# Performance work log

Hardware: AMD Instinct MI355X
Metric: run time of the kernel (lower is better)

The kernel has to match this reference:

```python
import jax, jax.numpy as jnp
import numpy as np
from jax import lax

N_EMBD = 4096
N_EXPERTS = 64


def setup_inputs() -> dict:
    key = jax.random.key(0)
    kx, kw = jax.random.split(key)
    x = jax.random.normal(kx, (4, 4096, N_EMBD), dtype=jnp.float32)
    # nn.Linear(n_embd, n_experts, bias=False) -> weight shape [n_experts, n_embd]
    W = jax.random.normal(kw, (N_EXPERTS, N_EMBD), dtype=jnp.float32) * (1.0 / np.sqrt(N_EMBD))
    return {"x": x, "W": W}


def reference(x, W):
    # logits = x @ W^T : [B, S, n_experts]
    logits = jnp.einsum('bsd,ed->bse', x, W)
    topk_vals, topk_idx = lax.top_k(logits, 2)  # [B, S, 2]
    gates = jax.nn.softmax(topk_vals, axis=-1)  # softmax over just the top-2 values
    return (topk_idx, gates)
```

## Files before the change

kernel.cpp:

```cpp
#include <hip/hip_runtime.h>
#include <math.h>

#define N_EMBD    4096
#define N_EXPERTS 64
#define N_TOKENS  16384
#define TAU       1e-3f
#define NT_BLK    32
#define KS        4
#define K_BLK     (N_EMBD / KS)
#define NT2       16

typedef __attribute__((ext_vector_type(8))) short bf16x8;
typedef __attribute__((ext_vector_type(4))) float f32x4;

#define MFMA16 __builtin_amdgcn_mfma_f32_16x16x32_bf16
#define PIN2(a, b) asm volatile("" :: "v"(a), "v"(b))

struct hl_pair { unsigned h, l; };

__device__ __forceinline__ hl_pair split_pair(float f0, float f1) {
    unsigned u0 = __builtin_bit_cast(unsigned, f0);
    unsigned u1 = __builtin_bit_cast(unsigned, f1);
    unsigned r0 = u0 + 0x7FFFu + ((u0 >> 16) & 1u);
    unsigned r1 = u1 + 0x7FFFu + ((u1 >> 16) & 1u);
    hl_pair p;
    p.h = (r0 >> 16) | (r1 & 0xFFFF0000u);
    float h0 = __builtin_bit_cast(float, r0 & 0xFFFF0000u);
    float h1 = __builtin_bit_cast(float, r1 & 0xFFFF0000u);
    float l0 = f0 - h0;
    float l1 = f1 - h1;
    unsigned v0 = __builtin_bit_cast(unsigned, l0);
    unsigned v1 = __builtin_bit_cast(unsigned, l1);
    unsigned s0 = v0 + 0x7FFFu + ((v0 >> 16) & 1u);
    unsigned s1 = v1 + 0x7FFFu + ((v1 >> 16) & 1u);
    p.l = (s0 >> 16) | (s1 & 0xFFFF0000u);
    return p;
}

__global__ void w_pack_bf16(const float* __restrict__ W,
                            uint4* __restrict__ Bpack,
                            int* __restrict__ flags) {
    int tid = blockIdx.x * blockDim.x + threadIdx.x;
    if (tid == 0) flags[0] = 0;
    int lane = tid & 63;
    int nt   = (tid >> 6) & 3;
    int ks   = tid >> 8;
    int e = nt * 16 + (lane & 15);
    int k = ks * 32 + ((lane >> 4) << 3);
    const float* src = W + (size_t)e * N_EMBD + k;
    uint4 hp, lp;
    hl_pair p0 = split_pair(src[0], src[1]);
    hl_pair p1 = split_pair(src[2], src[3]);
    hl_pair p2 = split_pair(src[4], src[5]);
    hl_pair p3 = split_pair(src[6], src[7]);
    hp.x = p0.h; lp.x = p0.l;
    hp.y = p1.h; lp.y = p1.l;
    hp.z = p2.h; lp.z = p2.l;
    hp.w = p3.h; lp.w = p3.l;
    size_t F = (size_t)ks * 8 + nt * 2;
    Bpack[F * 64 + lane]       = hp;
    Bpack[(F + 1) * 64 + lane] = lp;
}

__device__ __forceinline__ void store_split8(char* buf, int off, f32x4 a, f32x4 b) {
    hl_pair p0 = split_pair(a.x, a.y);
    hl_pair p1 = split_pair(a.z, a.w);
    hl_pair p2 = split_pair(b.x, b.y);
    hl_pair p3 = split_pair(b.z, b.w);
    uint4 h, l;
    h.x = p0.h; h.y = p1.h; h.z = p2.h; h.w = p3.h;
    l.x = p0.l; l.y = p1.l; l.z = p2.l; l.w = p3.l;
    *(uint4*)(buf + off)        = h;
    *(uint4*)(buf + off + 4096) = l;
}

__global__ __launch_bounds__(256, 4) void router_gemm(
        const float* __restrict__ x,
        const uint4* __restrict__ Bpack,
        float* __restrict__ partial) {
    __shared__ __align__(16) char ldsA[2 * 8192];

    const int tid  = threadIdx.x;
    const int lane = tid & 63;
    const int w    = tid >> 6;
    const int kq   = blockIdx.x & 3;
    const int tok0 = (blockIdx.x >> 2) * NT_BLK;
    const int l15 = lane & 15, l16 = lane >> 4;

    const int row_w = tid >> 3;
    const int c8    = tid & 7;
    const f32x4* g = (const f32x4*)(x + (size_t)(tok0 + row_w) * N_EMBD
                                      + kq * K_BLK + c8 * 8);
    const int wo = row_w * 128 + ((c8 * 16) ^ ((row_w & 7) << 4));

    const int swz_r = (l15 & 7) << 4;
    const int ro0 = l15 * 128 + ((l16 * 16)      ^ swz_r);
    const int ro1 = l15 * 128 + ((64 + l16 * 16) ^ swz_r);

    f32x4 acc0 = {0.f, 0.f, 0.f, 0.f};
    f32x4 acc1 = {0.f, 0.f, 0.f, 0.f};
    f32x4 ra0, ra1, rb0, rb1;

    char* buf0 = ldsA;
    char* buf1 = ldsA + 8192;

    const uint4* bbase = Bpack + ((size_t)(kq * 32) * 8 + w * 2) * 64 + lane;

#define LOADA(P, t) { P##0 = g[(t) * 16]; P##1 = g[(t) * 16 + 1]; }
#define STOREA(buf, P) store_split8(buf, wo, P##0, P##1)
#define COMPUTE(bufR, tt) {                                                   \
    const uint4* bq = bbase + (size_t)(tt) * 1024;                            \
    uint4 bh0q = bq[0];   uint4 bl0q = bq[64];                                \
    uint4 bh1q = bq[512]; uint4 bl1q = bq[576];                               \
    bf16x8 bh0 = __builtin_bit_cast(bf16x8, bh0q);                            \
    bf16x8 bl0 = __builtin_bit_cast(bf16x8, bl0q);                            \
    bf16x8 bh1 = __builtin_bit_cast(bf16x8, bh1q);                            \
    bf16x8 bl1 = __builtin_bit_cast(bf16x8, bl1q);                            \
    bf16x8 a;                                                                 \
    a = *(const bf16x8*)((bufR) + ro0);                                       \
    acc0 = MFMA16(a, bh0, acc0, 0, 0, 0);                                     \
    acc0 = MFMA16(a, bl0, acc0, 0, 0, 0);                                     \
    a = *(const bf16x8*)((bufR) + ro0 + 4096);                                \
    acc0 = MFMA16(a, bh0, acc0, 0, 0, 0);                                     \
    a = *(const bf16x8*)((bufR) + ro0 + 2048);                                \
    acc1 = MFMA16(a, bh0, acc1, 0, 0, 0);                                     \
    acc1 = MFMA16(a, bl0, acc1, 0, 0, 0);                                     \
    a = *(const bf16x8*)((bufR) + ro0 + 2048 + 4096);                         \
    acc1 = MFMA16(a, bh0, acc1, 0, 0, 0);                                     \
    a = *(const bf16x8*)((bufR) + ro1);                                       \
    acc0 = MFMA16(a, bh1, acc0, 0, 0, 0);                                     \
    acc0 = MFMA16(a, bl1, acc0, 0, 0, 0);                                     \
    a = *(const bf16x8*)((bufR) + ro1 + 4096);                                \
    acc0 = MFMA16(a, bh1, acc0, 0, 0, 0);                                     \
    a = *(const bf16x8*)((bufR) + ro1 + 2048);                                \
    acc1 = MFMA16(a, bh1, acc1, 0, 0, 0);                                     \
    acc1 = MFMA16(a, bl1, acc1, 0, 0, 0);                                     \
    a = *(const bf16x8*)((bufR) + ro1 + 2048 + 4096);                         \
    acc1 = MFMA16(a, bh1, acc1, 0, 0, 0);                                     \
}

    LOADA(rb, 0);
    STOREA(buf0, rb);
    LOADA(rb, 1);
    LOADA(ra, 2);
    PIN2(rb0, rb1);
    PIN2(ra0, ra1);
    asm volatile("s_waitcnt lgkmcnt(0)" ::: "memory");
    __builtin_amdgcn_s_barrier();
    __builtin_amdgcn_sched_barrier(0);

    for (int t = 0; t < NT2; t += 2) {
        COMPUTE(buf0, t);
        STOREA(buf1, rb);
        if (t + 3 < NT2) { LOADA(rb, t + 3); PIN2(rb0, rb1); }
        asm volatile("s_waitcnt lgkmcnt(0)" ::: "memory");
        __builtin_amdgcn_s_barrier();
        __builtin_amdgcn_sched_barrier(0);

        COMPUTE(buf1, t + 1);
        if (t + 2 < NT2) {
            STOREA(buf0, ra);
            if (t + 4 < NT2) { LOADA(ra, t + 4); PIN2(ra0, ra1); }
            asm volatile("s_waitcnt lgkmcnt(0)" ::: "memory");
            __builtin_amdgcn_s_barrier();
            __builtin_amdgcn_sched_barrier(0);
        }
    }
#undef LOADA
#undef STOREA
#undef COMPUTE

    float* po = partial + ((size_t)kq * N_TOKENS + tok0) * 64 + w * 16 + l15;
#pragma unroll
    for (int j = 0; j < 4; ++j) {
        po[(size_t)(l16 * 4 + j) * 64]      = acc0[j];
        po[(size_t)(16 + l16 * 4 + j) * 64] = acc1[j];
    }
}

__global__ void finalize(const float* __restrict__ partial,
                         float* __restrict__ out,
                         int* __restrict__ flags) {
    const int lane = threadIdx.x & 63;
    const int tok  = blockIdx.x * 4 + (threadIdx.x >> 6);

    float v = partial[(size_t)tok * 64 + lane]
            + partial[((size_t)N_TOKENS + tok) * 64 + lane]
            + partial[((size_t)2 * N_TOKENS + tok) * 64 + lane]
            + partial[((size_t)3 * N_TOKENS + tok) * 64 + lane];

    float m1 = v; int i1 = lane;
#pragma unroll
    for (int off = 32; off; off >>= 1) {
        float ov = __shfl_xor(m1, off); int oi = __shfl_xor(i1, off);
        if (ov > m1 || (ov == m1 && oi < i1)) { m1 = ov; i1 = oi; }
    }
    float m2 = (lane == i1) ? -INFINITY : v; int i2 = lane;
#pragma unroll
    for (int off = 32; off; off >>= 1) {
        float ov = __shfl_xor(m2, off); int oi = __shfl_xor(i2, off);
        if (ov > m2 || (ov == m2 && oi < i2)) { m2 = ov; i2 = oi; }
    }
    float m3 = (lane == i1 || lane == i2) ? -INFINITY : v;
#pragma unroll
    for (int off = 32; off; off >>= 1)
        m3 = fmaxf(m3, __shfl_xor(m3, off));

    if (lane == 0) {
        float e2  = __expf(m2 - m1);
        float inv = 1.0f / (1.0f + e2);
        float2 idx = make_float2((float)i1, (float)i2);
        float2 gts = make_float2(inv, e2 * inv);
        *(float2*)(out + 2 * tok) = idx;
        *(float2*)(out + 2 * N_TOKENS + 2 * tok) = gts;
        if ((m1 - m2 < TAU) || (m2 - m3 < TAU)) {
            int p = atomicAdd(flags, 1);
            if (p < N_TOKENS) flags[1 + p] = tok;
        }
    }
}

__global__ __launch_bounds__(256) void refine(const float* __restrict__ x,
                                              const float* __restrict__ W,
                                              const int* __restrict__ flags,
                                              float* __restrict__ out) {
    __shared__ double redd[64];
    const int lane = threadIdx.x & 63;
    const int wv   = threadIdx.x >> 6;
    int cnt = flags[0];
    if (cnt > N_TOKENS) cnt = N_TOKENS;

    for (int i = blockIdx.x; i < cnt; i += gridDim.x) {
        const int tok = flags[1 + i];
        const float4* xr4 = (const float4*)(x + (size_t)tok * N_EMBD);
#pragma unroll
        for (int ee = 0; ee < 16; ++ee) {
            const int e = wv * 16 + ee;
            const float4* wr = (const float4*)(W + (size_t)e * N_EMBD);
            double acc = 0.0;
#pragma unroll 4
            for (int c = 0; c < 16; ++c) {
                float4 xv = xr4[c * 64 + lane];
                float4 wq = wr[c * 64 + lane];
                acc += (double)xv.x * wq.x + (double)xv.y * wq.y
                     + (double)xv.z * wq.z + (double)xv.w * wq.w;
            }
#pragma unroll
            for (int off = 32; off; off >>= 1)
                acc += __shfl_xor(acc, off);
            if (lane == 0) redd[e] = acc;
        }
        __syncthreads();
        if (wv == 0) {
            double v = redd[lane];
            double m1 = v; int i1 = lane;
#pragma unroll
            for (int off = 32; off; off >>= 1) {
                double ov = __shfl_xor(m1, off); int oi = __shfl_xor(i1, off);
                if (ov > m1 || (ov == m1 && oi < i1)) { m1 = ov; i1 = oi; }
            }
            double m2 = (lane == i1) ? -INFINITY : v; int i2 = lane;
#pragma unroll
            for (int off = 32; off; off >>= 1) {
                double ov = __shfl_xor(m2, off); int oi = __shfl_xor(i2, off);
                if (ov > m2 || (ov == m2 && oi < i2)) { m2 = ov; i2 = oi; }
            }
            if (lane == 0) {
                double e2  = exp(m2 - m1);
                double inv = 1.0 / (1.0 + e2);
                out[2 * tok + 0] = (float)i1;
                out[2 * tok + 1] = (float)i2;
                out[2 * N_TOKENS + 2 * tok + 0] = (float)inv;
                out[2 * N_TOKENS + 2 * tok + 1] = (float)(e2 * inv);
            }
        }
        __syncthreads();
    }
}

extern "C" void kernel_launch(void* const* d_in, const int* in_sizes, int n_in,
                              void* d_out, int out_size, void* d_ws, size_t ws_size,
                              hipStream_t stream) {
    const float* x = (const float*)d_in[0];
    const float* W = (const float*)d_in[1];
    float* out = (float*)d_out;

    uint4* Bpack   = (uint4*)d_ws;
    int*   flags   = (int*)((char*)d_ws + (1u << 20));
    float* partial = (float*)((char*)d_ws + (2u << 20));

    w_pack_bf16<<<128, 256, 0, stream>>>(W, Bpack, flags);
    router_gemm<<<(N_TOKENS / NT_BLK) * KS, 256, 0, stream>>>(x, Bpack, partial);
    finalize   <<<N_TOKENS / 4, 256, 0, stream>>>(partial, out, flags);
    refine     <<<128, 256, 0, stream>>>(x, W, flags, out);
}
```

Baseline: 114.2 us.

## Prefetch B fragments one stage ahead and reduce A prefetch depth

Software-pipelines the packed weight (B) loads: B fragments for the next tile are issued into registers before the current tile's MFMAs, instead of being loaded inside the compute step. The A prefetch depth drops from two tiles ahead to one, and the register pinning asm is removed. The launch-bounds occupancy hint rises from 4 to 5 blocks per CU. The aim is to hide global-load latency for B behind compute and to allow more waves per CU. The risk is register spilling or stalls from the shallower A prefetch.

```diff
diff --git a/kernel.cpp b/kernel.cpp
--- a/kernel.cpp
+++ b/kernel.cpp
@@ -14,7 +14,6 @@
 typedef __attribute__((ext_vector_type(4))) float f32x4;
 
 #define MFMA16 __builtin_amdgcn_mfma_f32_16x16x32_bf16
-#define PIN2(a, b) asm volatile("" :: "v"(a), "v"(b))
 
 struct hl_pair { unsigned h, l; };
 
@@ -74,7 +73,7 @@
     *(uint4*)(buf + off + 4096) = l;
 }
 
-__global__ __launch_bounds__(256, 4) void router_gemm(
+__global__ __launch_bounds__(256, 5) void router_gemm(
         const float* __restrict__ x,
         const uint4* __restrict__ Bpack,
         float* __restrict__ partial) {
@@ -100,6 +99,8 @@
     f32x4 acc0 = {0.f, 0.f, 0.f, 0.f};
     f32x4 acc1 = {0.f, 0.f, 0.f, 0.f};
     f32x4 ra0, ra1, rb0, rb1;
+    uint4 bah0, bal0, bah1, bal1;
+    uint4 bbh0, bbl0, bbh1, bbl1;
 
     char* buf0 = ldsA;
     char* buf1 = ldsA + 8192;
@@ -107,15 +108,14 @@
     const uint4* bbase = Bpack + ((size_t)(kq * 32) * 8 + w * 2) * 64 + lane;
 
 #define LOADA(P, t) { P##0 = g[(t) * 16]; P##1 = g[(t) * 16 + 1]; }
+#define LOADB(P, tt) { const uint4* _q = bbase + (size_t)(tt) * 1024;         \
+    P##h0 = _q[0]; P##l0 = _q[64]; P##h1 = _q[512]; P##l1 = _q[576]; }
 #define STOREA(buf, P) store_split8(buf, wo, P##0, P##1)
-#define COMPUTE(bufR, tt) {                                                   \
-    const uint4* bq = bbase + (size_t)(tt) * 1024;                            \
-    uint4 bh0q = bq[0];   uint4 bl0q = bq[64];                                \
-    uint4 bh1q = bq[512]; uint4 bl1q = bq[576];                               \
-    bf16x8 bh0 = __builtin_bit_cast(bf16x8, bh0q);                            \
-    bf16x8 bl0 = __builtin_bit_cast(bf16x8, bl0q);                            \
-    bf16x8 bh1 = __builtin_bit_cast(bf16x8, bh1q);                            \
-    bf16x8 bl1 = __builtin_bit_cast(bf16x8, bl1q);                            \
+#define COMPUTE(bufR, B) {                                                    \
+    bf16x8 bh0 = __builtin_bit_cast(bf16x8, B##h0);                           \
+    bf16x8 bl0 = __builtin_bit_cast(bf16x8, B##l0);                           \
+    bf16x8 bh1 = __builtin_bit_cast(bf16x8, B##h1);                           \
+    bf16x8 bl1 = __builtin_bit_cast(bf16x8, B##l1);                           \
     bf16x8 a;                                                                 \
     a = *(const bf16x8*)((bufR) + ro0);                                       \
     acc0 = MFMA16(a, bh0, acc0, 0, 0, 0);                                     \
@@ -141,32 +141,38 @@
 
     LOADA(rb, 0);
     STOREA(buf0, rb);
-    LOADA(rb, 1);
-    LOADA(ra, 2);
-    PIN2(rb0, rb1);
-    PIN2(ra0, ra1);
+    LOADB(ba, 0);
+    LOADA(ra, 1);
+    __builtin_amdgcn_sched_barrier(0);
     asm volatile("s_waitcnt lgkmcnt(0)" ::: "memory");
     __builtin_amdgcn_s_barrier();
     __builtin_amdgcn_sched_barrier(0);
 
     for (int t = 0; t < NT2; t += 2) {
-        COMPUTE(buf0, t);
-        STOREA(buf1, rb);
-        if (t + 3 < NT2) { LOADA(rb, t + 3); PIN2(rb0, rb1); }
+        LOADB(bb, t + 1);
+        if (t + 2 < NT2) LOADA(rb, t + 2);
+        __builtin_amdgcn_sched_barrier(0);
+        COMPUTE(buf0, ba);
+        STOREA(buf1, ra);
         asm volatile("s_waitcnt lgkmcnt(0)" ::: "memory");
         __builtin_amdgcn_s_barrier();
         __builtin_amdgcn_sched_barrier(0);
 
-        COMPUTE(buf1, t + 1);
         if (t + 2 < NT2) {
-            STOREA(buf0, ra);
-            if (t + 4 < NT2) { LOADA(ra, t + 4); PIN2(ra0, ra1); }
+            LOADB(ba, t + 2);
+            if (t + 3 < NT2) LOADA(ra, t + 3);
+            __builtin_amdgcn_sched_barrier(0);
+            COMPUTE(buf1, bb);
+            STOREA(buf0, rb);
             asm volatile("s_waitcnt lgkmcnt(0)" ::: "memory");
             __builtin_amdgcn_s_barrier();
             __builtin_amdgcn_sched_barrier(0);
+        } else {
+            COMPUTE(buf1, bb);
         }
     }
 #undef LOADA
+#undef LOADB
 #undef STOREA
 #undef COMPUTE
 
```

Result: faster. 109.2 us (-4.4%).
